# Kernel optimization log

Hardware: AMD Instinct MI355X
Metric: run time of the kernel (lower is better)

The kernel has to match this reference:

```python
import jax, jax.numpy as jnp
import numpy as np

L, D, H, V, B, S = 12, 768, 12, 50257, 1, 2048
F = 4 * D
HD = D // H
EPS = 1e-5
NEG = -1e38


def setup_inputs() -> dict:
    key = jax.random.key(0)
    ks = jax.random.split(key, 12)
    s = 0.02
    f32 = jnp.float32
    return {
        "x": jax.random.normal(ks[0], (B, S, D), f32),
        "ln1_g": jnp.ones((L, D), f32), "ln1_b": jnp.zeros((L, D), f32),
        "Wq": jax.random.normal(ks[1], (L, D, D), f32) * s,
        "Wk": jax.random.normal(ks[2], (L, D, D), f32) * s,
        "Wv": jax.random.normal(ks[3], (L, D, D), f32) * s,
        "Wo": jax.random.normal(ks[4], (L, D, D), f32) * s,
        "bo": jnp.zeros((L, D), f32),
        "ln2_g": jnp.ones((L, D), f32), "ln2_b": jnp.zeros((L, D), f32),
        "Wfc": jax.random.normal(ks[5], (L, D, F), f32) * s,
        "bfc": jnp.zeros((L, F), f32),
        "Wp": jax.random.normal(ks[6], (L, F, D), f32) * s,
        "bp": jnp.zeros((L, D), f32),
        "lnf_g": jnp.ones((D,), f32), "lnf_b": jnp.zeros((D,), f32),
        "Wlm": jax.random.normal(ks[7], (D, V), f32) * s,
    }


def _ln(h, g, b):
    mu = h.mean(-1, keepdims=True)
    var = ((h - mu) ** 2).mean(-1, keepdims=True)
    return (h - mu) * jax.lax.rsqrt(var + EPS) * g + b


def reference(x, ln1_g, ln1_b, Wq, Wk, Wv, Wo, bo, ln2_g, ln2_b,
              Wfc, bfc, Wp, bp, lnf_g, lnf_b, Wlm):
    Bx, Sx, Dx = x.shape
    # additive causal mask, NOTE: original has no 1/sqrt(head_dim) scaling
    mask = (1.0 - jnp.tril(jnp.ones((Sx, Sx), x.dtype))) * NEG

    def block(h, p):
        g1, b1, wq, wk, wv, wo, bo_, g2, b2, wfc, bfc_, wp, bp_ = p
        hn = _ln(h, g1, b1)
        def heads(w):  # [B,S,D] -> [B,H,S,hd]
            return (hn @ w).reshape(Bx, Sx, H, HD).transpose(0, 2, 1, 3)
        q, k, v = heads(wq), heads(wk), heads(wv)
        scores = jnp.einsum('bhqd,bhkd->bhqk', q, k) + mask
        probs = jax.nn.softmax(scores, axis=-1)
        attn = jnp.einsum('bhqk,bhkd->bhqd', probs, v)
        attn = attn.transpose(0, 2, 1, 3).reshape(Bx, Sx, Dx)
        h = h + attn @ wo + bo_
        hn2 = _ln(h, g2, b2)
        ff = jax.nn.gelu(hn2 @ wfc + bfc_, approximate=False) @ wp + bp_
        return h + ff, None

    h, _ = jax.lax.scan(
        block, x,
        (ln1_g, ln1_b, Wq, Wk, Wv, Wo, bo, ln2_g, ln2_b, Wfc, bfc, Wp, bp))
    return _ln(h, lnf_g, lnf_b) @ Wlm
```

## Files before the change

### kernel.cpp

```cpp
#include <hip/hip_runtime.h>
#include <hip/hip_bf16.h>
#include <math.h>

typedef unsigned short ushort;
typedef __attribute__((ext_vector_type(8))) short short8;
typedef __attribute__((ext_vector_type(4))) short short4v;
typedef __attribute__((ext_vector_type(4))) float f4v;

constexpr int SEQ = 2048;
constexpr int DM  = 768;
constexpr int NH  = 12;
constexpr int HDM = 64;
constexpr int FF  = 3072;
constexpr int NL  = 12;
constexpr int NV  = 50257;
constexpr int NVP = 50496;

__device__ inline ushort f2bf(float f) {
    union { float f; unsigned u; } v; v.f = f;
    unsigned r = v.u + 0x7fffu + ((v.u >> 16) & 1u);
    return (ushort)(r >> 16);
}

__device__ __forceinline__ void gld16(const ushort* g, ushort* l) {
    __builtin_amdgcn_global_load_lds(
        (const __attribute__((address_space(1))) void*)g,
        (__attribute__((address_space(3))) void*)l, 16, 0, 0);
}

__global__ __launch_bounds__(256) void ln_kernel(const float* __restrict__ x,
                                                 const float* __restrict__ g,
                                                 const float* __restrict__ b,
                                                 ushort* __restrict__ out) {
    int row = blockIdx.x;
    int t = threadIdx.x;
    const float* xr = x + (size_t)row * DM;
    float v0 = xr[t], v1 = xr[t + 256], v2 = xr[t + 512];
    float s = v0 + v1 + v2;
    float s2 = v0 * v0 + v1 * v1 + v2 * v2;
    for (int m = 1; m < 64; m <<= 1) { s += __shfl_xor(s, m); s2 += __shfl_xor(s2, m); }
    __shared__ float ls[4], ls2[4];
    int w = t >> 6;
    if ((t & 63) == 0) { ls[w] = s; ls2[w] = s2; }
    __syncthreads();
    s = ls[0] + ls[1] + ls[2] + ls[3];
    s2 = ls2[0] + ls2[1] + ls2[2] + ls2[3];
    float mu = s * (1.0f / DM);
    float var = s2 * (1.0f / DM) - mu * mu;
    float rs = rsqrtf(var + 1e-5f);
    ushort* o = out + (size_t)row * DM;
    o[t]       = f2bf((v0 - mu) * rs * g[t]       + b[t]);
    o[t + 256] = f2bf((v1 - mu) * rs * g[t + 256] + b[t + 256]);
    o[t + 512] = f2bf((v2 - mu) * rs * g[t + 512] + b[t + 512]);
}

template <int NS>
__global__ __launch_bounds__(256) void ln_spk(const float* __restrict__ p,
                                              const float* __restrict__ bias,
                                              float* __restrict__ h,
                                              const float* __restrict__ g,
                                              const float* __restrict__ b,
                                              ushort* __restrict__ out) {
    int row = blockIdx.x;
    int t = threadIdx.x;
    size_t base = (size_t)row * DM;
    float v[3];
    #pragma unroll
    for (int j = 0; j < 3; ++j) {
        int col = t + j * 256;
        float acc = h[base + col] + bias[col];
        #pragma unroll
        for (int s = 0; s < NS; ++s) acc += p[(size_t)s * SEQ * DM + base + col];
        v[j] = acc;
        h[base + col] = acc;
    }
    float s1 = v[0] + v[1] + v[2];
    float s2 = v[0] * v[0] + v[1] * v[1] + v[2] * v[2];
    for (int m = 1; m < 64; m <<= 1) { s1 += __shfl_xor(s1, m); s2 += __shfl_xor(s2, m); }
    __shared__ float ls[4], ls2[4];
    int w = t >> 6;
    if ((t & 63) == 0) { ls[w] = s1; ls2[w] = s2; }
    __syncthreads();
    s1 = ls[0] + ls[1] + ls[2] + ls[3];
    s2 = ls2[0] + ls2[1] + ls2[2] + ls2[3];
    float mu = s1 * (1.0f / DM);
    float var = s2 * (1.0f / DM) - mu * mu;
    float rs = rsqrtf(var + 1e-5f);
    #pragma unroll
    for (int j = 0; j < 3; ++j) {
        int col = t + j * 256;
        out[base + col] = f2bf((v[j] - mu) * rs * g[col] + b[col]);
    }
}

struct CvtArgs {
    const float* src[7];
    ushort*      dst[7];
    long inL[7], outL[7];
    int  K[7], N[7], tk[7], tn[7];
    int  base[8];
};

__global__ __launch_bounds__(256) void cvt_all(CvtArgs a) {
    __shared__ ushort T[64][72];
    int idx = blockIdx.x;
    int seg = 0;
    #pragma unroll
    for (int i = 1; i < 7; ++i) if (idx >= a.base[i]) seg = i;
    int local = idx - a.base[seg];
    int K = a.K[seg], N = a.N[seg];
    int tk = a.tk[seg], tn = a.tn[seg];
    int k_t = local % tk;
    int rst = local / tk;
    int n_t = rst % tn;
    int l   = rst / tn;
    const float* ip = a.src[seg] + (size_t)l * a.inL[seg];
    ushort* op      = a.dst[seg] + (size_t)l * a.outL[seg];
    int kb = k_t * 64, nb = n_t * 64;
    int t = threadIdx.x;
    int nl = t & 63, ks = (t >> 6) * 16;
    int n = nb + nl;
    #pragma unroll
    for (int j = 0; j < 16; ++j) {
        float f = (n < N) ? ip[(size_t)(kb + ks + j) * N + n] : 0.f;
        T[nl][ks + j] = f2bf(f);
    }
    __syncthreads();
    int r = t >> 2, c4 = (t & 3) * 16;
    *(short8*)(op + (size_t)(nb + r) * K + kb + c4)     = *(const short8*)&T[r][c4];
    *(short8*)(op + (size_t)(nb + r) * K + kb + c4 + 8) = *(const short8*)&T[r][c4 + 8];
}

template <int BM, int BN, int EPI, bool DB, bool SWZ, int MINW>
__global__ __launch_bounds__(256, MINW) void gemmT(const ushort* __restrict__ A,
                                                   const ushort* __restrict__ Bt,
                                                   const float* __restrict__ bias,
                                                   const float* __restrict__ res,
                                                   void* __restrict__ outp,
                                                   ushort* __restrict__ vt,
                                                   int M, int N, int K,
                                                   int kLen, int ldOut) {
    constexpr int FM = BM / 32;
    constexpr int FN = BN / 32;
    constexpr int NBUF = DB ? 2 : 1;
    constexpr int ASZ = BM * 64;
    constexpr int BSZ = BN * 64;
    __shared__ ushort As[NBUF * ASZ];
    __shared__ ushort Bs[NBUF * BSZ];
    int tid = threadIdx.x, lane = tid & 63, wave = tid >> 6;
    int wm = (wave >> 1) * (BM / 2), wn = (wave & 1) * (BN / 2);
    int mBase, nBase;
    if constexpr (SWZ) {
        int gx = gridDim.x;
        int nwg = gx * gridDim.y;
        int flat = blockIdx.y * gx + blockIdx.x;
        int xcd = flat & 7, idx = flat >> 3;
        int q = nwg >> 3, r = nwg & 7;
        int wg = (xcd < r ? xcd * (q + 1) : r * (q + 1) + (xcd - r) * q) + idx;
        mBase = (wg % gx) * BM;
        nBase = (wg / gx) * BN;
    } else {
        mBase = blockIdx.x * BM;
        nBase = blockIdx.y * BN;
    }
    int kOff = kLen * blockIdx.z;
    int lr = lane & 15, lg = lane >> 4;
    int swz = (lr & 7) << 3;

    f4v acc[FM][FN];
    #pragma unroll
    for (int i = 0; i < FM; ++i)
        #pragma unroll
        for (int j = 0; j < FN; ++j) acc[i][j] = (f4v){0.f, 0.f, 0.f, 0.f};

    int cBase = wave * 64 + lane;

    auto stage = [&](int kb, int buf) {
        #pragma unroll
        for (int i = 0; i < BM / 32; ++i) {
            int c = i * 256 + cBase;
            int row = c >> 3;
            int kc = (c & 7) ^ (row & 7);
            gld16(A + (size_t)(mBase + row) * K + kOff + kb + kc * 8,
                  As + buf * ASZ + (size_t)(i * 256 + wave * 64) * 8);
        }
        #pragma unroll
        for (int i = 0; i < BN / 32; ++i) {
            int c = i * 256 + cBase;
            int row = c >> 3;
            int kc = (c & 7) ^ (row & 7);
            gld16(Bt + (size_t)(nBase + row) * K + kOff + kb + kc * 8,
                  Bs + buf * BSZ + (size_t)(i * 256 + wave * 64) * 8);
        }
    };
    auto compute = [&](int buf) {
        #pragma unroll
        for (int kk = 0; kk < 2; ++kk) {
            short8 a[FM], b[FN];
            #pragma unroll
            for (int fr = 0; fr < FM; ++fr)
                a[fr] = *(const short8*)(As + buf * ASZ + (wm + fr * 16 + lr) * 64 + ((((kk * 4 + lg) << 3)) ^ swz));
            #pragma unroll
            for (int fc = 0; fc < FN; ++fc)
                b[fc] = *(const short8*)(Bs + buf * BSZ + (wn + fc * 16 + lr) * 64 + ((((kk * 4 + lg) << 3)) ^ swz));
            #pragma unroll
            for (int fr = 0; fr < FM; ++fr)
                #pragma unroll
                for (int fc = 0; fc < FN; ++fc)
                    acc[fr][fc] = __builtin_amdgcn_mfma_f32_16x16x32_bf16(a[fr], b[fc], acc[fr][fc], 0, 0, 0);
        }
    };

    if constexpr (DB) {
        stage(0, 0);
        __syncthreads();
        int cur = 0;
        for (int kb = 0; kb < kLen; kb += 64) {
            if (kb + 64 < kLen) stage(kb + 64, cur ^ 1);
            compute(cur);
            __syncthreads();
            cur ^= 1;
        }
    } else {
        for (int kb = 0; kb < kLen; kb += 64) {
            stage(kb, 0);
            __syncthreads();
            compute(0);
            __syncthreads();
        }
    }

    if constexpr (EPI == 4) {
        if (nBase < 1536) {
            #pragma unroll
            for (int fr = 0; fr < FM; ++fr)
                #pragma unroll
                for (int fc = 0; fc < FN; ++fc)
                    #pragma unroll
                    for (int r = 0; r < 4; ++r) {
                        int row = mBase + wm + fr * 16 + 4 * lg + r;
                        int col = nBase + wn + fc * 16 + lr;
                        ((ushort*)outp)[(size_t)row * ldOut + col] = f2bf(acc[fr][fc][r]);
                    }
        } else {
            #pragma unroll
            for (int fr = 0; fr < FM; ++fr)
                #pragma unroll
                for (int fc = 0; fc < FN; ++fc) {
                    short4v pk;
                    #pragma unroll
                    for (int r = 0; r < 4; ++r) pk[r] = (short)f2bf(acc[fr][fc][r]);
                    int d  = nBase - 1536 + wn + fc * 16 + lr;
                    int m0 = mBase + wm + fr * 16 + 4 * lg;
                    *(short4v*)(vt + (size_t)d * SEQ + m0) = pk;
                }
        }
        return;
    }

    float* out3 = (float*)outp;
    if constexpr (EPI == 3) out3 += (size_t)blockIdx.z * M * ldOut;

    #pragma unroll
    for (int fr = 0; fr < FM; ++fr)
        #pragma unroll
        for (int fc = 0; fc < FN; ++fc)
            #pragma unroll
            for (int r = 0; r < 4; ++r) {
                int row = mBase + wm + fr * 16 + 4 * lg + r;
                int col = nBase + wn + fc * 16 + lr;
                float v = acc[fr][fc][r];
                if constexpr (EPI == 0) {
                    ((ushort*)outp)[(size_t)row * ldOut + col] = f2bf(v);
                } else if constexpr (EPI == 1) {
                    v += bias[col] + res[(size_t)row * ldOut + col];
                    ((float*)outp)[(size_t)row * ldOut + col] = v;
                } else if constexpr (EPI == 2) {
                    v += bias[col];
                    v = 0.5f * v * (1.f + erff(v * 0.70710678118f));
                    ((ushort*)outp)[(size_t)row * ldOut + col] = f2bf(v);
                } else {
                    if (col < N) out3[(size_t)row * ldOut + col] = v;
                }
            }
}

__global__ __launch_bounds__(128) void attn_v7(const ushort* __restrict__ Qg,
                                               const ushort* __restrict__ Kg,
                                               const ushort* __restrict__ Vt,
                                               ushort* __restrict__ Og) {
    __shared__ ushort Ks[2 * 4096];
    __shared__ ushort Vs[2 * 4096];
    __shared__ ushort Ps[2 * 1024];
    int tid = threadIdx.x, lane = tid & 63, wave = tid >> 6;
    int flat = blockIdx.x;
    int qt   = (SEQ / 32) - 1 - (flat / NH);
    int head = flat % NH;
    int lr = lane & 15, lg = lane >> 4;
    int qr0 = qt * 32 + wave * 16;
    int hoff = head * HDM;
    int swz = (lr & 7) << 3;
    int ktiles = (qt * 32 + 31) / 64 + 1;

    short8 qf0 = *(const short8*)(Qg + (size_t)(qr0 + lr) * 2304 + hoff + lg * 8);
    short8 qf1 = *(const short8*)(Qg + (size_t)(qr0 + lr) * 2304 + hoff + 32 + lg * 8);

    const f4v fz = {0.f, 0.f, 0.f, 0.f};
    f4v o[4];
    o[0] = fz; o[1] = fz; o[2] = fz; o[3] = fz;
    float mrow[4] = {-1e30f, -1e30f, -1e30f, -1e30f};
    float lsum[4] = {0.f, 0.f, 0.f, 0.f};

    auto stageKV = [&](int kb, int buf) {
        #pragma unroll
        for (int j = 0; j < 4; ++j) {
            int cc = j * 128 + wave * 64 + lane;
            int row = cc >> 3;
            int kc = (cc & 7) ^ (row & 7);
            gld16(Kg + (size_t)(kb * 64 + row) * 2304 + hoff + kc * 8,
                  Ks + buf * 4096 + (size_t)(j * 128 + wave * 64) * 8);
            gld16(Vt + (size_t)(hoff + row) * SEQ + kb * 64 + kc * 8,
                  Vs + buf * 4096 + (size_t)(j * 128 + wave * 64) * 8);
        }
    };

    stageKV(0, 0);
    __syncthreads();
    int cur = 0;

    for (int kb = 0; kb < ktiles; ++kb) {
        if (kb + 1 < ktiles) stageKV(kb + 1, cur ^ 1);

        f4v s[4];
        #pragma unroll
        for (int n = 0; n < 4; ++n) {
            const ushort* kr = Ks + cur * 4096 + (n * 16 + lr) * 64;
            short8 k0 = *(const short8*)(kr + ((lg << 3) ^ swz));
            short8 k1 = *(const short8*)(kr + ((((4 + lg) << 3)) ^ swz));
            f4v z = fz;
            z = __builtin_amdgcn_mfma_f32_16x16x32_bf16(qf0, k0, z, 0, 0, 0);
            s[n] = __builtin_amdgcn_mfma_f32_16x16x32_bf16(qf1, k1, z, 0, 0, 0);
        }
        if (kb == ktiles - 1) {
            #pragma unroll
            for (int n = 0; n < 4; ++n)
                #pragma unroll
                for (int r = 0; r < 4; ++r) {
                    int col = kb * 64 + n * 16 + lr;
                    int row = qr0 + 4 * lg + r;
                    if (col > row) s[n][r] = -1e38f;
                }
        }

        int sub = lr & 7, hi = lr >> 3;
        #pragma unroll
        for (int r = 0; r < 4; ++r) {
            float mx = fmaxf(fmaxf(s[0][r], s[1][r]), fmaxf(s[2][r], s[3][r]));
            mx = fmaxf(mx, __shfl_xor(mx, 1));
            mx = fmaxf(mx, __shfl_xor(mx, 2));
            mx = fmaxf(mx, __shfl_xor(mx, 4));
            mx = fmaxf(mx, __shfl_xor(mx, 8));
            float mnew = fmaxf(mrow[r], mx);
            float corr = __expf(mrow[r] - mnew);
            float ps0 = __expf(s[0][r] - mnew);
            float ps1 = __expf(s[1][r] - mnew);
            float ps2 = __expf(s[2][r] - mnew);
            float ps3 = __expf(s[3][r] - mnew);
            float rs = ps0 + ps1 + ps2 + ps3;
            rs += __shfl_xor(rs, 1);
            rs += __shfl_xor(rs, 2);
            rs += __shfl_xor(rs, 4);
            rs += __shfl_xor(rs, 8);
            lsum[r] = lsum[r] * corr + rs;
            mrow[r] = mnew;
            o[0][r] *= corr; o[1][r] *= corr; o[2][r] *= corr; o[3][r] *= corr;
            int prow = 4 * lg + r;
            ushort* pb = Ps + wave * 1024 + prow * 64;
            int px = prow & 7;
            pb[(((0 + hi) ^ px) << 3) | sub] = f2bf(ps0);
            pb[(((2 + hi) ^ px) << 3) | sub] = f2bf(ps1);
            pb[(((4 + hi) ^ px) << 3) | sub] = f2bf(ps2);
            pb[(((6 + hi) ^ px) << 3) | sub] = f2bf(ps3);
        }
        __syncthreads();

        #pragma unroll
        for (int kk = 0; kk < 2; ++kk) {
            short8 pa = *(const short8*)(Ps + wave * 1024 + lr * 64 + ((((kk * 4 + lg) << 3)) ^ swz));
            #pragma unroll
            for (int dn = 0; dn < 4; ++dn) {
                short8 vb = *(const short8*)(Vs + cur * 4096 + (dn * 16 + lr) * 64 + ((((kk * 4 + lg) << 3)) ^ swz));
                o[dn] = __builtin_amdgcn_mfma_f32_16x16x32_bf16(pa, vb, o[dn], 0, 0, 0);
            }
        }
        __syncthreads();
        cur ^= 1;
    }

    #pragma unroll
    for (int dn = 0; dn < 4; ++dn)
        #pragma unroll
        for (int r = 0; r < 4; ++r) {
            int row = qr0 + 4 * lg + r;
            Og[(size_t)row * DM + hoff + dn * 16 + lr] = f2bf(o[dn][r] / lsum[r]);
        }
}

template <int EPI>
__global__ __launch_bounds__(256) void gemm64(const ushort* __restrict__ A,
                                              const float* __restrict__ B,
                                              const float* __restrict__ bias,
                                              const float* __restrict__ res,
                                              void* __restrict__ outp,
                                              int M, int N, int K) {
    __shared__ ushort As[64][64];
    __shared__ ushort Bs[64][72];
    int tid = threadIdx.x;
    int lane = tid & 63, wave = tid >> 6;
    int wm = (wave >> 1) * 32, wn = (wave & 1) * 32;
    int mBase = blockIdx.x * 64, nBase = blockIdx.y * 64;
    int lr = lane & 15, lg = lane >> 4;

    const f4v fz = {0.f, 0.f, 0.f, 0.f};
    f4v acc[2][2];
    acc[0][0] = fz; acc[0][1] = fz; acc[1][0] = fz; acc[1][1] = fz;

    int ar = tid >> 2, ac = (tid & 3) * 16;
    int br = tid >> 2, bc = (tid & 3) * 16;

    for (int kb = 0; kb < K; kb += 64) {
        const short8* ag = (const short8*)(A + (size_t)(mBase + ar) * K + kb + ac);
        *(short8*)&As[ar][ac]     = ag[0];
        *(short8*)&As[ar][ac + 8] = ag[1];
        if constexpr (EPI == 3) {
            #pragma unroll
            for (int j = 0; j < 16; ++j) {
                int col = nBase + bc + j;
                float f = (col < N) ? B[(size_t)(kb + br) * N + col] : 0.f;
                Bs[bc + j][br] = f2bf(f);
            }
        } else {
            const float4* bg = (const float4*)(B + (size_t)(kb + br) * N + nBase + bc);
            float fv[16];
            *(float4*)&fv[0]  = bg[0];
            *(float4*)&fv[4]  = bg[1];
            *(float4*)&fv[8]  = bg[2];
            *(float4*)&fv[12] = bg[3];
            #pragma unroll
            for (int j = 0; j < 16; ++j) Bs[bc + j][br] = f2bf(fv[j]);
        }
        __syncthreads();
        #pragma unroll
        for (int kk = 0; kk < 2; ++kk) {
            short8 a0 = *(const short8*)&As[wm + lr][kk * 32 + lg * 8];
            short8 a1 = *(const short8*)&As[wm + 16 + lr][kk * 32 + lg * 8];
            short8 b0 = *(const short8*)&Bs[wn + lr][kk * 32 + lg * 8];
            short8 b1 = *(const short8*)&Bs[wn + 16 + lr][kk * 32 + lg * 8];
            acc[0][0] = __builtin_amdgcn_mfma_f32_16x16x32_bf16(a0, b0, acc[0][0], 0, 0, 0);
            acc[0][1] = __builtin_amdgcn_mfma_f32_16x16x32_bf16(a0, b1, acc[0][1], 0, 0, 0);
            acc[1][0] = __builtin_amdgcn_mfma_f32_16x16x32_bf16(a1, b0, acc[1][0], 0, 0, 0);
            acc[1][1] = __builtin_amdgcn_mfma_f32_16x16x32_bf16(a1, b1, acc[1][1], 0, 0, 0);
        }
        __syncthreads();
    }

    #pragma unroll
    for (int fm = 0; fm < 2; ++fm)
        #pragma unroll
        for (int fn = 0; fn < 2; ++fn)
            #pragma unroll
            for (int r = 0; r < 4; ++r) {
                int row = mBase + wm + fm * 16 + 4 * lg + r;
                int col = nBase + wn + fn * 16 + lr;
                float v = acc[fm][fn][r];
                if constexpr (EPI == 0) {
                    ((ushort*)outp)[(size_t)row * N + col] = f2bf(v);
                } else if constexpr (EPI == 1) {
                    v += bias[col] + res[(size_t)row * N + col];
                    ((float*)outp)[(size_t)row * N + col] = v;
                } else if constexpr (EPI == 2) {
                    v += bias[col];
                    v = 0.5f * v * (1.f + erff(v * 0.70710678118f));
                    ((ushort*)outp)[(size_t)row * N + col] = f2bf(v);
                } else {
                    if (col < N) ((float*)outp)[(size_t)row * N + col] = v;
                }
            }
}

__global__ __launch_bounds__(256) void attn_stage(const ushort* __restrict__ Qg,
                                                  const ushort* __restrict__ Kg,
                                                  const ushort* __restrict__ Vg,
                                                  ushort* __restrict__ Og,
                                                  int ld) {
    __shared__ ushort Ks[64][64];
    __shared__ ushort Vs[64][72];
    __shared__ ushort Ps[4][16][64];
    int tid = threadIdx.x, lane = tid & 63, wave = tid >> 6;
    int qb = blockIdx.x, head = blockIdx.y;
    int lr = lane & 15, lg = lane >> 4;
    int qr0 = qb * 64 + wave * 16;
    size_t hoff = (size_t)head * HDM;

    short8 qf0 = *(const short8*)(Qg + (size_t)(qr0 + lr) * ld + hoff + lg * 8);
    short8 qf1 = *(const short8*)(Qg + (size_t)(qr0 + lr) * ld + hoff + 32 + lg * 8);

    const f4v fz = {0.f, 0.f, 0.f, 0.f};
    f4v o[4];
    o[0] = fz; o[1] = fz; o[2] = fz; o[3] = fz;
    float mrow[4] = {-1e30f, -1e30f, -1e30f, -1e30f};
    float lsum[4] = {0.f, 0.f, 0.f, 0.f};

    int r_ = tid >> 2, c_ = (tid & 3) * 16;

    for (int kb = 0; kb <= qb; ++kb) {
        const short8* kg = (const short8*)(Kg + (size_t)(kb * 64 + r_) * ld + hoff + c_);
        *(short8*)&Ks[r_][c_]     = kg[0];
        *(short8*)&Ks[r_][c_ + 8] = kg[1];
        const short8* vg = (const short8*)(Vg + (size_t)(kb * 64 + r_) * ld + hoff + c_);
        short8 v0 = vg[0], v1 = vg[1];
        #pragma unroll
        for (int j = 0; j < 8; ++j) {
            Vs[c_ + j][r_]     = (ushort)v0[j];
            Vs[c_ + 8 + j][r_] = (ushort)v1[j];
        }
        __syncthreads();

        f4v s[4];
        #pragma unroll
        for (int n = 0; n < 4; ++n) {
            short8 k0 = *(const short8*)&Ks[n * 16 + lr][lg * 8];
            short8 k1 = *(const short8*)&Ks[n * 16 + lr][32 + lg * 8];
            f4v z = fz;
            z = __builtin_amdgcn_mfma_f32_16x16x32_bf16(qf0, k0, z, 0, 0, 0);
            s[n] = __builtin_amdgcn_mfma_f32_16x16x32_bf16(qf1, k1, z, 0, 0, 0);
        }
        if (kb == qb) {
            #pragma unroll
            for (int n = 0; n < 4; ++n)
                #pragma unroll
                for (int r = 0; r < 4; ++r) {
                    int col = kb * 64 + n * 16 + lr;
                    int row = qr0 + 4 * lg + r;
                    if (col > row) s[n][r] = -1e38f;
                }
        }

        #pragma unroll
        for (int r = 0; r < 4; ++r) {
            float mx = fmaxf(fmaxf(s[0][r], s[1][r]), fmaxf(s[2][r], s[3][r]));
            mx = fmaxf(mx, __shfl_xor(mx, 1));
            mx = fmaxf(mx, __shfl_xor(mx, 2));
            mx = fmaxf(mx, __shfl_xor(mx, 4));
            mx = fmaxf(mx, __shfl_xor(mx, 8));
            float mnew = fmaxf(mrow[r], mx);
            float corr = __expf(mrow[r] - mnew);
            float ps0 = __expf(s[0][r] - mnew);
            float ps1 = __expf(s[1][r] - mnew);
            float ps2 = __expf(s[2][r] - mnew);
            float ps3 = __expf(s[3][r] - mnew);
            float rs = ps0 + ps1 + ps2 + ps3;
            rs += __shfl_xor(rs, 1);
            rs += __shfl_xor(rs, 2);
            rs += __shfl_xor(rs, 4);
            rs += __shfl_xor(rs, 8);
            lsum[r] = lsum[r] * corr + rs;
            mrow[r] = mnew;
            o[0][r] *= corr; o[1][r] *= corr; o[2][r] *= corr; o[3][r] *= corr;
            Ps[wave][4 * lg + r][0 * 16 + lr] = f2bf(ps0);
            Ps[wave][4 * lg + r][1 * 16 + lr] = f2bf(ps1);
            Ps[wave][4 * lg + r][2 * 16 + lr] = f2bf(ps2);
            Ps[wave][4 * lg + r][3 * 16 + lr] = f2bf(ps3);
        }
        __syncthreads();

        #pragma unroll
        for (int kk = 0; kk < 2; ++kk) {
            short8 pa = *(const short8*)&Ps[wave][lr][kk * 32 + lg * 8];
            #pragma unroll
            for (int dn = 0; dn < 4; ++dn) {
                short8 vb = *(const short8*)&Vs[dn * 16 + lr][kk * 32 + lg * 8];
                o[dn] = __builtin_amdgcn_mfma_f32_16x16x32_bf16(pa, vb, o[dn], 0, 0, 0);
            }
        }
        __syncthreads();
    }

    #pragma unroll
    for (int dn = 0; dn < 4; ++dn)
        #pragma unroll
        for (int r = 0; r < 4; ++r) {
            int row = qr0 + 4 * lg + r;
            Og[(size_t)row * DM + hoff + dn * 16 + lr] = f2bf(o[dn][r] / lsum[r]);
        }
}

extern "C" void kernel_launch(void* const* d_in, const int* in_sizes, int n_in,
                              void* d_out, int out_size, void* d_ws, size_t ws_size,
                              hipStream_t stream) {
    const float* x     = (const float*)d_in[0];
    const float* ln1_g = (const float*)d_in[1];
    const float* ln1_b = (const float*)d_in[2];
    const float* Wq    = (const float*)d_in[3];
    const float* Wk    = (const float*)d_in[4];
    const float* Wv    = (const float*)d_in[5];
    const float* Wo    = (const float*)d_in[6];
    const float* bo    = (const float*)d_in[7];
    const float* ln2_g = (const float*)d_in[8];
    const float* ln2_b = (const float*)d_in[9];
    const float* Wfc   = (const float*)d_in[10];
    const float* bfc   = (const float*)d_in[11];
    const float* Wp    = (const float*)d_in[12];
    const float* bp    = (const float*)d_in[13];
    const float* lnf_g = (const float*)d_in[14];
    const float* lnf_b = (const float*)d_in[15];
    const float* Wlm   = (const float*)d_in[16];

    dim3 blk(256);

    size_t offs[13];
    size_t need = 0;
    size_t sizes[12] = {
        (size_t)SEQ * DM * 4,
        (size_t)SEQ * DM * 2,
        (size_t)SEQ * 2304 * 2,
        (size_t)SEQ * DM * 2,
        (size_t)SEQ * FF * 2,
        (size_t)DM * SEQ * 2,
        (size_t)NL * 2304 * DM * 2,
        (size_t)NL * DM * DM * 2,
        (size_t)NL * FF * DM * 2,
        (size_t)NL * DM * FF * 2,
        (size_t)NVP * DM * 2,
        (size_t)4 * SEQ * DM * 4,
    };
    for (int i = 0; i < 12; ++i) { offs[i] = need; need += sizes[i]; }
    offs[12] = need;
    size_t need_base = offs[11];
    bool useSpk = (ws_size >= need);

    if (ws_size >= need_base) {
        char* ws = (char*)d_ws;
        float*  h    = (float*)(ws + offs[0]);
        ushort* hn   = (ushort*)(ws + offs[1]);
        ushort* qkv  = (ushort*)(ws + offs[2]);
        ushort* ab_  = (ushort*)(ws + offs[3]);
        ushort* fb_  = (ushort*)(ws + offs[4]);
        ushort* vt   = (ushort*)(ws + offs[5]);
        ushort* qkvw = (ushort*)(ws + offs[6]);
        ushort* wow  = (ushort*)(ws + offs[7]);
        ushort* fcw  = (ushort*)(ws + offs[8]);
        ushort* wpw  = (ushort*)(ws + offs[9]);
        ushort* lmw  = (ushort*)(ws + offs[10]);
        float*  spk  = (float*)(ws + offs[11]);

        hipMemcpyAsync(h, x, (size_t)SEQ * DM * 4, hipMemcpyDeviceToDevice, stream);

        CvtArgs ca;
        const float* srcs[7] = {Wq, Wk, Wv, Wo, Wfc, Wp, Wlm};
        ushort* dsts[7] = {qkvw, qkvw + DM * DM, qkvw + 2 * DM * DM, wow, fcw, wpw, lmw};
        long inLs[7]  = {(long)DM * DM, (long)DM * DM, (long)DM * DM, (long)DM * DM,
                         (long)DM * FF, (long)FF * DM, 0};
        long outLs[7] = {(long)2304 * DM, (long)2304 * DM, (long)2304 * DM, (long)DM * DM,
                         (long)FF * DM, (long)DM * FF, 0};
        int Ks_[7] = {DM, DM, DM, DM, DM, FF, DM};
        int Ns_[7] = {DM, DM, DM, DM, FF, DM, NV};
        int tks[7] = {12, 12, 12, 12, 12, 48, 12};
        int tns[7] = {12, 12, 12, 12, 48, 12, NVP / 64};
        int lays[7] = {NL, NL, NL, NL, NL, NL, 1};
        int total = 0;
        for (int i = 0; i < 7; ++i) {
            ca.src[i] = srcs[i]; ca.dst[i] = dsts[i];
            ca.inL[i] = inLs[i]; ca.outL[i] = outLs[i];
            ca.K[i] = Ks_[i]; ca.N[i] = Ns_[i]; ca.tk[i] = tks[i]; ca.tn[i] = tns[i];
            ca.base[i] = total;
            total += tks[i] * tns[i] * lays[i];
        }
        ca.base[7] = total;
        cvt_all<<<dim3(total), blk, 0, stream>>>(ca);

        ln_kernel<<<SEQ, blk, 0, stream>>>(h, ln1_g, ln1_b, hn);
        for (int l = 0; l < NL; ++l) {
            const ushort* qw = qkvw + (size_t)l * 2304 * DM;
            gemmT<64, 64, 4, true, false, 2><<<dim3(32, 36), blk, 0, stream>>>(hn, qw, nullptr, nullptr, qkv, vt, SEQ, 2304, DM, DM, 2304);
            attn_v7<<<dim3((SEQ / 32) * NH), dim3(128), 0, stream>>>(qkv, qkv + 768, vt, ab_);
            if (useSpk) {
                gemmT<64, 64, 3, true, false, 2><<<dim3(32, 12, 2), blk, 0, stream>>>(ab_, wow + (size_t)l * DM * DM, nullptr, nullptr, spk, nullptr, SEQ, DM, DM, DM / 2, DM);
                ln_spk<2><<<SEQ, blk, 0, stream>>>(spk, bo + l * DM, h, ln2_g + l * DM, ln2_b + l * DM, hn);
            } else {
                gemmT<64, 64, 1, true, false, 2><<<dim3(32, 12), blk, 0, stream>>>(ab_, wow + (size_t)l * DM * DM, bo + l * DM, h, h, nullptr, SEQ, DM, DM, DM, DM);
                ln_kernel<<<SEQ, blk, 0, stream>>>(h, ln2_g + l * DM, ln2_b + l * DM, hn);
            }
            gemmT<64, 64, 2, true, false, 2><<<dim3(32, 48), blk, 0, stream>>>(hn, fcw + (size_t)l * FF * DM, bfc + l * FF, nullptr, fb_, nullptr, SEQ, FF, DM, DM, FF);
            const float* g2 = (l + 1 < NL) ? ln1_g + (l + 1) * DM : lnf_g;
            const float* b2 = (l + 1 < NL) ? ln1_b + (l + 1) * DM : lnf_b;
            if (useSpk) {
                gemmT<64, 64, 3, true, false, 2><<<dim3(32, 12, 4), blk, 0, stream>>>(fb_, wpw + (size_t)l * DM * FF, nullptr, nullptr, spk, nullptr, SEQ, DM, FF, FF / 4, DM);
                ln_spk<4><<<SEQ, blk, 0, stream>>>(spk, bp + l * DM, h, g2, b2, hn);
            } else {
                gemmT<64, 64, 1, true, false, 2><<<dim3(32, 12), blk, 0, stream>>>(fb_, wpw + (size_t)l * DM * FF, bp + l * DM, h, h, nullptr, SEQ, DM, FF, FF, DM);
                ln_kernel<<<SEQ, blk, 0, stream>>>(h, g2, b2, hn);
            }
        }
        gemmT<128, 192, 3, false, true, 3><<<dim3(16, NVP / 192), blk, 0, stream>>>(hn, lmw, nullptr, nullptr, d_out, nullptr, SEQ, NV, DM, DM, NV);
        return;
    }

    char* ws = (char*)d_ws;
    float*  h   = (float*)ws;   ws += (size_t)SEQ * DM * 4;
    ushort* hn  = (ushort*)ws;  ws += (size_t)SEQ * DM * 2;
    ushort* qb_ = (ushort*)ws;  ws += (size_t)SEQ * DM * 2;
    ushort* kb_ = (ushort*)ws;  ws += (size_t)SEQ * DM * 2;
    ushort* vb_ = (ushort*)ws;  ws += (size_t)SEQ * DM * 2;
    ushort* ab_ = (ushort*)ws;  ws += (size_t)SEQ * DM * 2;
    ushort* fb_ = (ushort*)ws;  ws += (size_t)SEQ * FF * 2;

    hipMemcpyAsync(h, x, (size_t)SEQ * DM * 4, hipMemcpyDeviceToDevice, stream);

    dim3 gdd(SEQ / 64, DM / 64);
    dim3 gdf(SEQ / 64, FF / 64);
    dim3 gda(SEQ / 64, NH);
    dim3 gdl(SEQ / 64, (NV + 63) / 64);

    for (int l = 0; l < NL; ++l) {
        ln_kernel<<<SEQ, blk, 0, stream>>>(h, ln1_g + l * DM, ln1_b + l * DM, hn);
        gemm64<0><<<gdd, blk, 0, stream>>>(hn, Wq + (size_t)l * DM * DM, nullptr, nullptr, qb_, SEQ, DM, DM);
        gemm64<0><<<gdd, blk, 0, stream>>>(hn, Wk + (size_t)l * DM * DM, nullptr, nullptr, kb_, SEQ, DM, DM);
        gemm64<0><<<gdd, blk, 0, stream>>>(hn, Wv + (size_t)l * DM * DM, nullptr, nullptr, vb_, SEQ, DM, DM);
        attn_stage<<<gda, blk, 0, stream>>>(qb_, kb_, vb_, ab_, DM);
        gemm64<1><<<gdd, blk, 0, stream>>>(ab_, Wo + (size_t)l * DM * DM, bo + l * DM, h, h, SEQ, DM, DM);
        ln_kernel<<<SEQ, blk, 0, stream>>>(h, ln2_g + l * DM, ln2_b + l * DM, hn);
        gemm64<2><<<gdf, blk, 0, stream>>>(hn, Wfc + (size_t)l * DM * FF, bfc + l * FF, nullptr, fb_, SEQ, FF, DM);
        gemm64<1><<<gdd, blk, 0, stream>>>(fb_, Wp + (size_t)l * FF * DM, bp + l * DM, h, h, SEQ, DM, FF);
    }
    ln_kernel<<<SEQ, blk, 0, stream>>>(h, lnf_g, lnf_b, hn);
    gemm64<3><<<gdl, blk, 0, stream>>>(hn, Wlm, nullptr, nullptr, d_out, SEQ, NV, DM);
}
```

Before: 2.359 ms.

## Enlarge attention query tile to 64 rows so each wave processes two fragments

The attention kernel now gives each block 64 query rows instead of 32, and each wave handles two 16-row fragments. Every K/V tile staged into shared memory and read into registers is then reused across twice as many query rows, which halves global K/V traffic and staging per query. In exchange the grid shrinks to 384 blocks, which lowers parallelism and may leave compute units idle on a large GPU. Register pressure also rises from the doubled accumulators and score fragments.

```diff
diff --git a/kernel.cpp b/kernel.cpp
--- a/kernel.cpp
+++ b/kernel.cpp
@@ -285,31 +285,40 @@
             }
 }
 
-__global__ __launch_bounds__(128) void attn_v7(const ushort* __restrict__ Qg,
+__global__ __launch_bounds__(128) void attn_v8(const ushort* __restrict__ Qg,
                                                const ushort* __restrict__ Kg,
                                                const ushort* __restrict__ Vt,
                                                ushort* __restrict__ Og) {
     __shared__ ushort Ks[2 * 4096];
     __shared__ ushort Vs[2 * 4096];
-    __shared__ ushort Ps[2 * 1024];
+    __shared__ ushort Ps[4 * 1024];
     int tid = threadIdx.x, lane = tid & 63, wave = tid >> 6;
     int flat = blockIdx.x;
-    int qt   = (SEQ / 32) - 1 - (flat / NH);
+    int qt   = (SEQ / 64) - 1 - (flat / NH);
     int head = flat % NH;
     int lr = lane & 15, lg = lane >> 4;
-    int qr0 = qt * 32 + wave * 16;
+    int qr0 = qt * 64 + wave * 32;
     int hoff = head * HDM;
     int swz = (lr & 7) << 3;
-    int ktiles = (qt * 32 + 31) / 64 + 1;
-
-    short8 qf0 = *(const short8*)(Qg + (size_t)(qr0 + lr) * 2304 + hoff + lg * 8);
-    short8 qf1 = *(const short8*)(Qg + (size_t)(qr0 + lr) * 2304 + hoff + 32 + lg * 8);
+    int ktiles = qt + 1;
+
+    short8 qf[2][2];
+    #pragma unroll
+    for (int f = 0; f < 2; ++f) {
+        const ushort* qr = Qg + (size_t)(qr0 + f * 16 + lr) * 2304 + hoff;
+        qf[f][0] = *(const short8*)(qr + lg * 8);
+        qf[f][1] = *(const short8*)(qr + 32 + lg * 8);
+    }
 
     const f4v fz = {0.f, 0.f, 0.f, 0.f};
-    f4v o[4];
-    o[0] = fz; o[1] = fz; o[2] = fz; o[3] = fz;
-    float mrow[4] = {-1e30f, -1e30f, -1e30f, -1e30f};
-    float lsum[4] = {0.f, 0.f, 0.f, 0.f};
+    f4v o[2][4];
+    float mrow[2][4], lsum[2][4];
+    #pragma unroll
+    for (int f = 0; f < 2; ++f)
+        #pragma unroll
+        for (int r = 0; r < 4; ++r) {
+            o[f][r] = fz; mrow[f][r] = -1e30f; lsum[f][r] = 0.f;
+        }
 
     auto stageKV = [&](int kb, int buf) {
         #pragma unroll
@@ -331,66 +340,82 @@
     for (int kb = 0; kb < ktiles; ++kb) {
         if (kb + 1 < ktiles) stageKV(kb + 1, cur ^ 1);
 
-        f4v s[4];
+        short8 k0[4], k1[4];
         #pragma unroll
         for (int n = 0; n < 4; ++n) {
             const ushort* kr = Ks + cur * 4096 + (n * 16 + lr) * 64;
-            short8 k0 = *(const short8*)(kr + ((lg << 3) ^ swz));
-            short8 k1 = *(const short8*)(kr + ((((4 + lg) << 3)) ^ swz));
-            f4v z = fz;
-            z = __builtin_amdgcn_mfma_f32_16x16x32_bf16(qf0, k0, z, 0, 0, 0);
-            s[n] = __builtin_amdgcn_mfma_f32_16x16x32_bf16(qf1, k1, z, 0, 0, 0);
-        }
+            k0[n] = *(const short8*)(kr + ((lg << 3) ^ swz));
+            k1[n] = *(const short8*)(kr + ((((4 + lg) << 3)) ^ swz));
+        }
+
+        f4v s[2][4];
+        #pragma unroll
+        for (int f = 0; f < 2; ++f)
+            #pragma unroll
+            for (int n = 0; n < 4; ++n) {
+                f4v z = fz;
+                z = __builtin_amdgcn_mfma_f32_16x16x32_bf16(qf[f][0], k0[n], z, 0, 0, 0);
+                s[f][n] = __builtin_amdgcn_mfma_f32_16x16x32_bf16(qf[f][1], k1[n], z, 0, 0, 0);
+            }
         if (kb == ktiles - 1) {
             #pragma unroll
-            for (int n = 0; n < 4; ++n)
+            for (int f = 0; f < 2; ++f)
                 #pragma unroll
-                for (int r = 0; r < 4; ++r) {
-                    int col = kb * 64 + n * 16 + lr;
-                    int row = qr0 + 4 * lg + r;
-                    if (col > row) s[n][r] = -1e38f;
-                }
+                for (int n = 0; n < 4; ++n)
+                    #pragma unroll
+                    for (int r = 0; r < 4; ++r) {
+                        int col = kb * 64 + n * 16 + lr;
+                        int row = qr0 + f * 16 + 4 * lg + r;
+                        if (col > row) s[f][n][r] = -1e38f;
+                    }
         }
 
         int sub = lr & 7, hi = lr >> 3;
         #pragma unroll
-        for (int r = 0; r < 4; ++r) {
-            float mx = fmaxf(fmaxf(s[0][r], s[1][r]), fmaxf(s[2][r], s[3][r]));
-            mx = fmaxf(mx, __shfl_xor(mx, 1));
-            mx = fmaxf(mx, __shfl_xor(mx, 2));
-            mx = fmaxf(mx, __shfl_xor(mx, 4));
-            mx = fmaxf(mx, __shfl_xor(mx, 8));
-            float mnew = fmaxf(mrow[r], mx);
-            float corr = __expf(mrow[r] - mnew);
-            float ps0 = __expf(s[0][r] - mnew);
-            float ps1 = __expf(s[1][r] - mnew);
-            float ps2 = __expf(s[2][r] - mnew);
-            float ps3 = __expf(s[3][r] - mnew);
-            float rs = ps0 + ps1 + ps2 + ps3;
-            rs += __shfl_xor(rs, 1);
-            rs += __shfl_xor(rs, 2);
-            rs += __shfl_xor(rs, 4);
-            rs += __shfl_xor(rs, 8);
-            lsum[r] = lsum[r] * corr + rs;
-            mrow[r] = mnew;
-            o[0][r] *= corr; o[1][r] *= corr; o[2][r] *= corr; o[3][r] *= corr;
-            int prow = 4 * lg + r;
-            ushort* pb = Ps + wave * 1024 + prow * 64;
-            int px = prow & 7;
-            pb[(((0 + hi) ^ px) << 3) | sub] = f2bf(ps0);
-            pb[(((2 + hi) ^ px) << 3) | sub] = f2bf(ps1);
-            pb[(((4 + hi) ^ px) << 3) | sub] = f2bf(ps2);
-            pb[(((6 + hi) ^ px) << 3) | sub] = f2bf(ps3);
-        }
+        for (int f = 0; f < 2; ++f)
+            #pragma unroll
+            for (int r = 0; r < 4; ++r) {
+                float mx = fmaxf(fmaxf(s[f][0][r], s[f][1][r]), fmaxf(s[f][2][r], s[f][3][r]));
+                mx = fmaxf(mx, __shfl_xor(mx, 1));
+                mx = fmaxf(mx, __shfl_xor(mx, 2));
+                mx = fmaxf(mx, __shfl_xor(mx, 4));
+                mx = fmaxf(mx, __shfl_xor(mx, 8));
+                float mnew = fmaxf(mrow[f][r], mx);
+                float corr = __expf(mrow[f][r] - mnew);
+                float ps0 = __expf(s[f][0][r] - mnew);
+                float ps1 = __expf(s[f][1][r] - mnew);
+                float ps2 = __expf(s[f][2][r] - mnew);
+                float ps3 = __expf(s[f][3][r] - mnew);
+                float rs = ps0 + ps1 + ps2 + ps3;
+                rs += __shfl_xor(rs, 1);
+                rs += __shfl_xor(rs, 2);
+                rs += __shfl_xor(rs, 4);
+                rs += __shfl_xor(rs, 8);
+                lsum[f][r] = lsum[f][r] * corr + rs;
+                mrow[f][r] = mnew;
+                o[f][0][r] *= corr; o[f][1][r] *= corr; o[f][2][r] *= corr; o[f][3][r] *= corr;
+                int prow = 4 * lg + r;
+                ushort* pb = Ps + (wave * 2 + f) * 1024 + prow * 64;
+                int px = prow & 7;
+                pb[(((0 + hi) ^ px) << 3) | sub] = f2bf(ps0);
+                pb[(((2 + hi) ^ px) << 3) | sub] = f2bf(ps1);
+                pb[(((4 + hi) ^ px) << 3) | sub] = f2bf(ps2);
+                pb[(((6 + hi) ^ px) << 3) | sub] = f2bf(ps3);
+            }
         __syncthreads();
 
         #pragma unroll
         for (int kk = 0; kk < 2; ++kk) {
-            short8 pa = *(const short8*)(Ps + wave * 1024 + lr * 64 + ((((kk * 4 + lg) << 3)) ^ swz));
+            short8 pa[2];
+            #pragma unroll
+            for (int f = 0; f < 2; ++f)
+                pa[f] = *(const short8*)(Ps + (wave * 2 + f) * 1024 + lr * 64 + ((((kk * 4 + lg) << 3)) ^ swz));
             #pragma unroll
             for (int dn = 0; dn < 4; ++dn) {
                 short8 vb = *(const short8*)(Vs + cur * 4096 + (dn * 16 + lr) * 64 + ((((kk * 4 + lg) << 3)) ^ swz));
-                o[dn] = __builtin_amdgcn_mfma_f32_16x16x32_bf16(pa, vb, o[dn], 0, 0, 0);
+                #pragma unroll
+                for (int f = 0; f < 2; ++f)
+                    o[f][dn] = __builtin_amdgcn_mfma_f32_16x16x32_bf16(pa[f], vb, o[f][dn], 0, 0, 0);
             }
         }
         __syncthreads();
@@ -398,12 +423,14 @@
     }
 
     #pragma unroll
-    for (int dn = 0; dn < 4; ++dn)
-        #pragma unroll
-        for (int r = 0; r < 4; ++r) {
-            int row = qr0 + 4 * lg + r;
-            Og[(size_t)row * DM + hoff + dn * 16 + lr] = f2bf(o[dn][r] / lsum[r]);
-        }
+    for (int f = 0; f < 2; ++f)
+        #pragma unroll
+        for (int dn = 0; dn < 4; ++dn)
+            #pragma unroll
+            for (int r = 0; r < 4; ++r) {
+                int row = qr0 + f * 16 + 4 * lg + r;
+                Og[(size_t)row * DM + hoff + dn * 16 + lr] = f2bf(o[f][dn][r] / lsum[f][r]);
+            }
 }
 
 template <int EPI>
@@ -683,7 +710,7 @@
         for (int l = 0; l < NL; ++l) {
             const ushort* qw = qkvw + (size_t)l * 2304 * DM;
             gemmT<64, 64, 4, true, false, 2><<<dim3(32, 36), blk, 0, stream>>>(hn, qw, nullptr, nullptr, qkv, vt, SEQ, 2304, DM, DM, 2304);
-            attn_v7<<<dim3((SEQ / 32) * NH), dim3(128), 0, stream>>>(qkv, qkv + 768, vt, ab_);
+            attn_v8<<<dim3((SEQ / 64) * NH), dim3(128), 0, stream>>>(qkv, qkv + 768, vt, ab_);
             if (useSpk) {
                 gemmT<64, 64, 3, true, false, 2><<<dim3(32, 12, 2), blk, 0, stream>>>(ab_, wow + (size_t)l * DM * DM, nullptr, nullptr, spk, nullptr, SEQ, DM, DM, DM / 2, DM);
                 ln_spk<2><<<SEQ, blk, 0, stream>>>(spk, bo + l * DM, h, ln2_g + l * DM, ln2_b + l * DM, hn);
```

New measurement: 2.735 ms. 15.9% more time.

## Load V fragments directly from global and triple-buffer K to drop trailing barrier

Applied to the files above, without the earlier changes.

The attention kernel no longer stages V tiles in shared memory. Each lane loads its V MFMA operands straight from the transposed V buffer in global memory into registers. K staging moves to a three-slot rotating buffer so the barrier after the PV step can be removed. This cuts LDS traffic and one block-wide sync per key tile, at the cost of more registers and uncached global loads whose latency may not be fully hidden.

```diff
diff --git a/kernel.cpp b/kernel.cpp
--- a/kernel.cpp
+++ b/kernel.cpp
@@ -285,12 +285,11 @@
             }
 }
 
-__global__ __launch_bounds__(128) void attn_v7(const ushort* __restrict__ Qg,
+__global__ __launch_bounds__(128) void attn_v9(const ushort* __restrict__ Qg,
                                                const ushort* __restrict__ Kg,
                                                const ushort* __restrict__ Vt,
                                                ushort* __restrict__ Og) {
-    __shared__ ushort Ks[2 * 4096];
-    __shared__ ushort Vs[2 * 4096];
+    __shared__ ushort Ks[3 * 4096];
     __shared__ ushort Ps[2 * 1024];
     int tid = threadIdx.x, lane = tid & 63, wave = tid >> 6;
     int flat = blockIdx.x;
@@ -311,7 +310,7 @@
     float mrow[4] = {-1e30f, -1e30f, -1e30f, -1e30f};
     float lsum[4] = {0.f, 0.f, 0.f, 0.f};
 
-    auto stageKV = [&](int kb, int buf) {
+    auto stageK = [&](int kb, int buf) {
         #pragma unroll
         for (int j = 0; j < 4; ++j) {
             int cc = j * 128 + wave * 64 + lane;
@@ -319,17 +318,15 @@
             int kc = (cc & 7) ^ (row & 7);
             gld16(Kg + (size_t)(kb * 64 + row) * 2304 + hoff + kc * 8,
                   Ks + buf * 4096 + (size_t)(j * 128 + wave * 64) * 8);
-            gld16(Vt + (size_t)(hoff + row) * SEQ + kb * 64 + kc * 8,
-                  Vs + buf * 4096 + (size_t)(j * 128 + wave * 64) * 8);
         }
     };
 
-    stageKV(0, 0);
+    stageK(0, 0);
     __syncthreads();
-    int cur = 0;
+    int cur = 0, nxt = 1;
 
     for (int kb = 0; kb < ktiles; ++kb) {
-        if (kb + 1 < ktiles) stageKV(kb + 1, cur ^ 1);
+        if (kb + 1 < ktiles) stageK(kb + 1, nxt);
 
         f4v s[4];
         #pragma unroll
@@ -341,6 +338,14 @@
             z = __builtin_amdgcn_mfma_f32_16x16x32_bf16(qf0, k0, z, 0, 0, 0);
             s[n] = __builtin_amdgcn_mfma_f32_16x16x32_bf16(qf1, k1, z, 0, 0, 0);
         }
+
+        short8 vb[2][4];
+        #pragma unroll
+        for (int kk = 0; kk < 2; ++kk)
+            #pragma unroll
+            for (int dn = 0; dn < 4; ++dn)
+                vb[kk][dn] = *(const short8*)(Vt + (size_t)(hoff + dn * 16 + lr) * SEQ + kb * 64 + kk * 32 + lg * 8);
+
         if (kb == ktiles - 1) {
             #pragma unroll
             for (int n = 0; n < 4; ++n)
@@ -388,13 +393,11 @@
         for (int kk = 0; kk < 2; ++kk) {
             short8 pa = *(const short8*)(Ps + wave * 1024 + lr * 64 + ((((kk * 4 + lg) << 3)) ^ swz));
             #pragma unroll
-            for (int dn = 0; dn < 4; ++dn) {
-                short8 vb = *(const short8*)(Vs + cur * 4096 + (dn * 16 + lr) * 64 + ((((kk * 4 + lg) << 3)) ^ swz));
-                o[dn] = __builtin_amdgcn_mfma_f32_16x16x32_bf16(pa, vb, o[dn], 0, 0, 0);
-            }
-        }
-        __syncthreads();
-        cur ^= 1;
+            for (int dn = 0; dn < 4; ++dn)
+                o[dn] = __builtin_amdgcn_mfma_f32_16x16x32_bf16(pa, vb[kk][dn], o[dn], 0, 0, 0);
+        }
+        cur = nxt;
+        nxt = nxt + 1 == 3 ? 0 : nxt + 1;
     }
 
     #pragma unroll
@@ -683,7 +686,7 @@
         for (int l = 0; l < NL; ++l) {
             const ushort* qw = qkvw + (size_t)l * 2304 * DM;
             gemmT<64, 64, 4, true, false, 2><<<dim3(32, 36), blk, 0, stream>>>(hn, qw, nullptr, nullptr, qkv, vt, SEQ, 2304, DM, DM, 2304);
-            attn_v7<<<dim3((SEQ / 32) * NH), dim3(128), 0, stream>>>(qkv, qkv + 768, vt, ab_);
+            attn_v9<<<dim3((SEQ / 32) * NH), dim3(128), 0, stream>>>(qkv, qkv + 768, vt, ab_);
             if (useSpk) {
                 gemmT<64, 64, 3, true, false, 2><<<dim3(32, 12, 2), blk, 0, stream>>>(ab_, wow + (size_t)l * DM * DM, nullptr, nullptr, spk, nullptr, SEQ, DM, DM, DM / 2, DM);
                 ln_spk<2><<<SEQ, blk, 0, stream>>>(spk, bo + l * DM, h, ln2_g + l * DM, ln2_b + l * DM, hn);
```

After: 2.337 ms, median of 2. No clear change (-0.9%).
